# Performance work log

Hardware: AMD Instinct MI355X
Metric: run time of the kernel (lower is better)

## Reference

```python
import jax, jax.numpy as jnp
import numpy as np

IN_DIM = 300   # args.glove_init == 1
MID_DIM = 450  # ceil(1.5 * 300)
BATCH = 131072
NEG_SLOPE = 0.1


def setup_inputs() -> dict:
    key = jax.random.key(0)
    ks = jax.random.split(key, 13)

    def W(k, o, i):
        return jax.random.normal(k, (o, i), jnp.float32) * (1.0 / np.sqrt(i).astype(np.float32))

    def b(k, o):
        return jax.random.normal(k, (o,), jnp.float32) * 0.01

    inp = {"x": jax.random.normal(ks[0], (BATCH, IN_DIM), jnp.float32)}
    # NOT_op: Linear(300->450), LeakyReLU(0.1), Linear(450->300), LeakyReLU(0.1)
    inp["not_W1"] = W(ks[1], MID_DIM, IN_DIM);      inp["not_b1"] = b(ks[2], MID_DIM)
    inp["not_W2"] = W(ks[3], IN_DIM, MID_DIM);      inp["not_b2"] = b(ks[4], IN_DIM)
    # AND_op: Linear(600->450), LeakyReLU, Linear(450->300), LeakyReLU
    inp["and_W1"] = W(ks[5], MID_DIM, 2 * IN_DIM);  inp["and_b1"] = b(ks[6], MID_DIM)
    inp["and_W2"] = W(ks[7], IN_DIM, MID_DIM);      inp["and_b2"] = b(ks[8], IN_DIM)
    # OR_op: same shapes as AND_op
    inp["or_W1"] = W(ks[9], MID_DIM, 2 * IN_DIM);   inp["or_b1"] = b(ks[10], MID_DIM)
    inp["or_W2"] = W(ks[11], IN_DIM, MID_DIM);      inp["or_b2"] = b(ks[12], IN_DIM)
    inp["epoch"] = 1  # epoch <= el_epochs -> el_forward path
    return inp


def _mlp(x, W1, b1, W2, b2):
    # torch Linear: y = x @ W.T + b; LeakyReLU(0.1)
    h = jax.nn.leaky_relu(x @ W1.T + b1, NEG_SLOPE)
    return jax.nn.leaky_relu(h @ W2.T + b2, NEG_SLOPE)


def reference(x, not_W1, not_b1, not_W2, not_b2,
              and_W1, and_b1, and_W2, and_b2,
              or_W1, or_b1, or_W2, or_b2, epoch):
    # el_forward, fully batched (original loops over samples):
    # pairs: (x, NOT(NOT(x))), (x, AND([x,x])), (x, OR([x,x])); MSE over all pairs.
    s2a = _mlp(_mlp(x, not_W1, not_b1, not_W2, not_b2), not_W1, not_b1, not_W2, not_b2)
    xx = jnp.concatenate([x, x], axis=-1)  # [B, 600]
    s2b = _mlp(xx, and_W1, and_b1, and_W2, and_b2)
    s2c = _mlp(xx, or_W1, or_b1, or_W2, or_b2)
    # mean over the stacked 3B pairs == mean of the three per-pair MSEs
    loss = (jnp.mean((x - s2a) ** 2)
            + jnp.mean((x - s2b) ** 2)
            + jnp.mean((x - s2c) ** 2)) / 3.0
    return loss
```

## Files before the change

kernel.cpp:

```cpp
#include <hip/hip_runtime.h>

typedef __attribute__((ext_vector_type(8))) short short8;
typedef __attribute__((ext_vector_type(4))) float f32x4;

#define BATCH   131072
#define IND     300
#define MIDD    450
#define XS      328
#define HS      488
#define WXS     320
#define WHS     480
#define BM      96
#define NTHR    512
#define NBLK    ((BATCH + BM - 1) / BM)
#define MM      (BM / 16)

constexpr int SZ1 = 464 * WXS;
constexpr int SZ2 = 304 * WHS;
constexpr int O_NOT1 = 0;
constexpr int O_NOT2 = SZ1;
constexpr int O_AND1 = SZ1 + SZ2;
constexpr int O_AND2 = 2 * SZ1 + SZ2;
constexpr int O_OR1  = 2 * SZ1 + 2 * SZ2;
constexpr int O_OR2  = 3 * SZ1 + 2 * SZ2;
constexpr int WS_ELEMS = 3 * SZ1 + 3 * SZ2;

constexpr int XBYTES = BM * XS * 2;
constexpr int HBYTES = BM * HS * 2;
constexpr int LDS_BYTES = XBYTES + HBYTES;

__device__ __forceinline__ unsigned short f2b(float f) {
  unsigned u = __builtin_bit_cast(unsigned, f);
  u = (u + 0x7FFFu + ((u >> 16) & 1u)) >> 16;
  return (unsigned short)u;
}
__device__ __forceinline__ float b2f(unsigned short h) {
  unsigned u = ((unsigned)h) << 16;
  return __builtin_bit_cast(float, u);
}
__device__ __forceinline__ f32x4 mfma16(short8 a, short8 b, f32x4 c) {
  asm("v_mfma_f32_16x16x32_bf16 %0, %1, %2, %0" : "+v"(c) : "v"(a), "v"(b));
  return c;
}

__global__ void prep_weights(const float* __restrict__ nw1, const float* __restrict__ nw2,
                             const float* __restrict__ aw1, const float* __restrict__ aw2,
                             const float* __restrict__ ow1, const float* __restrict__ ow2,
                             unsigned short* __restrict__ ws)
{
  int idx = blockIdx.x * 256 + threadIdx.x;
  if (idx < 3 * SZ1) {
    int r = idx / SZ1, off = idx % SZ1;
    int n = off / WXS, k = off % WXS;
    float v = 0.f;
    if (n < MIDD && k < IND) {
      if (r == 0) v = nw1[n * IND + k];
      else {
        const float* s = (r == 1) ? aw1 : ow1;
        v = s[n * 2 * IND + k] + s[n * 2 * IND + IND + k];
      }
    }
    int base = (r == 0) ? O_NOT1 : (r == 1) ? O_AND1 : O_OR1;
    ws[base + off] = f2b(v);
  } else if (idx < WS_ELEMS) {
    int i2 = idx - 3 * SZ1;
    int r = i2 / SZ2, off = i2 % SZ2;
    int n = off / WHS, k = off % WHS;
    float v = 0.f;
    if (n < IND && k < MIDD) {
      const float* s = (r == 0) ? nw2 : (r == 1) ? aw2 : ow2;
      v = s[n * MIDD + k];
    }
    int base = (r == 0) ? O_NOT2 : (r == 1) ? O_AND2 : O_OR2;
    ws[base + off] = f2b(v);
  }
}

template <int KB, int NT, int N, bool MSE>
__device__ __forceinline__ void stage(const unsigned short* __restrict__ IN, int in_stride,
                                      const unsigned short* __restrict__ Wg, int wg_stride,
                                      const float* __restrict__ bias,
                                      unsigned short* __restrict__ Hout,
                                      const unsigned short* __restrict__ XT,
                                      float& sq, int rows, int tid, int wn, int l16, int lhi)
{
  constexpr int NJ = (NT + 7) / 8;
  f32x4 acc[MM][NJ];
#pragma unroll
  for (int m = 0; m < MM; m++)
#pragma unroll
    for (int j = 0; j < NJ; j++) acc[m][j] = f32x4{0.f, 0.f, 0.f, 0.f};

  const unsigned short* ap[MM];
#pragma unroll
  for (int m = 0; m < MM; m++) ap[m] = IN + (m * 16 + l16) * in_stride + lhi * 8;
  const unsigned short* bp[NJ];
#pragma unroll
  for (int j = 0; j < NJ; j++) {
    int nt = wn + 8 * j;
    int row = (nt < NT ? nt : 0) * 16 + l16;
    bp[j] = Wg + row * wg_stride + lhi * 8;
  }

  short8 a0[MM], a1[MM], b0[NJ], b1[NJ], b2[NJ];

#define LA_(buf, kk)                                                     \
  { _Pragma("unroll") for (int m = 0; m < MM; m++)                       \
      buf[m] = *(const short8*)(ap[m] + (kk) * 32); }
#define LB_(buf, kk)                                                     \
  { _Pragma("unroll") for (int j = 0; j < NJ; j++)                       \
      if (wn + 8 * j < NT) buf[j] = *(const short8*)(bp[j] + (kk) * 32); }

  LB_(b0, 0);
  LB_(b1, 1);
  LA_(a0, 0);

#pragma unroll
  for (int kb = 0; kb < KB; kb++) {
    short8* ac = (kb & 1) ? a1 : a0;
    short8* an = (kb & 1) ? a0 : a1;
    short8* bc = (kb % 3 == 0) ? b0 : (kb % 3 == 1) ? b1 : b2;
    short8* bn = ((kb + 2) % 3 == 0) ? b0 : ((kb + 2) % 3 == 1) ? b1 : b2;
    if (kb + 2 < KB) LB_(bn, kb + 2);
    if (kb + 1 < KB) LA_(an, kb + 1);
    __builtin_amdgcn_s_setprio(1);
#pragma unroll
    for (int j = 0; j < NJ; j++) {
      if (wn + 8 * j < NT) {
#pragma unroll
        for (int m = 0; m < MM; m++) acc[m][j] = mfma16(ac[m], bc[j], acc[m][j]);
      }
    }
    __builtin_amdgcn_s_setprio(0);
  }
#undef LA_
#undef LB_

  if (!MSE) __syncthreads();

#pragma unroll
  for (int j = 0; j < NJ; j++) {
    int nt = wn + 8 * j;
    if (nt >= NT) continue;
    int col = nt * 16 + l16;
    bool valid = col < N;
    float bv = valid ? bias[col] : 0.f;
#pragma unroll
    for (int m = 0; m < MM; m++) {
#pragma unroll
      for (int r = 0; r < 4; r++) {
        int row = m * 16 + lhi * 4 + r;
        float v = acc[m][j][r] + bv;
        v = v > 0.f ? v : 0.1f * v;
        if (MSE) {
          if (valid && row < rows) { float d = b2f(XT[row * XS + col]) - v; sq += d * d; }
        } else {
          if (valid) Hout[row * HS + col] = f2b(v);
        }
      }
    }
  }
  if (!MSE && N == IND) {
    for (int i = tid; i < BM * 20; i += NTHR) {
      int r = i / 20, c = i - r * 20;
      Hout[r * HS + IND + c] = 0;
    }
  }
}

__global__ __launch_bounds__(NTHR)
void fused(const float* __restrict__ x, const unsigned short* __restrict__ ws,
           const float* __restrict__ nb1, const float* __restrict__ nb2,
           const float* __restrict__ ab1, const float* __restrict__ ab2,
           const float* __restrict__ ob1, const float* __restrict__ ob2,
           float* __restrict__ out)
{
  extern __shared__ __align__(16) char smem[];
  unsigned short* X = (unsigned short*)smem;
  unsigned short* H = (unsigned short*)(smem + XBYTES);
  __shared__ float wsum[8];
  int tid = threadIdx.x, wid = tid >> 6, lane = tid & 63;
  int l16 = lane & 15, lhi = lane >> 4;

  for (int i = tid; i < LDS_BYTES / 4; i += NTHR) ((unsigned*)smem)[i] = 0u;
  __syncthreads();

  int row0 = blockIdx.x * BM;
  int rows = (row0 + BM <= BATCH) ? BM : (BATCH - row0);
  for (int i = tid; i < rows * IND; i += NTHR) {
    int r = i / IND, c = i - r * IND;
    X[r * XS + c] = f2b(x[(size_t)(row0 + r) * IND + c]);
  }
  __syncthreads();

  float sq = 0.f;
  stage<10, 29, MIDD, false>(X, XS, ws + O_NOT1, WXS, nb1, H, X, sq, rows, tid, wid, l16, lhi);
  __syncthreads();
  stage<15, 19, IND,  false>(H, HS, ws + O_NOT2, WHS, nb2, H, X, sq, rows, tid, wid, l16, lhi);
  __syncthreads();
  stage<10, 29, MIDD, false>(H, HS, ws + O_NOT1, WXS, nb1, H, X, sq, rows, tid, wid, l16, lhi);
  __syncthreads();
  stage<15, 19, IND,  true >(H, HS, ws + O_NOT2, WHS, nb2, H, X, sq, rows, tid, wid, l16, lhi);
  __syncthreads();
  stage<10, 29, MIDD, false>(X, XS, ws + O_AND1, WXS, ab1, H, X, sq, rows, tid, wid, l16, lhi);
  __syncthreads();
  stage<15, 19, IND,  true >(H, HS, ws + O_AND2, WHS, ab2, H, X, sq, rows, tid, wid, l16, lhi);
  __syncthreads();
  stage<10, 29, MIDD, false>(X, XS, ws + O_OR1,  WXS, ob1, H, X, sq, rows, tid, wid, l16, lhi);
  __syncthreads();
  stage<15, 19, IND,  true >(H, HS, ws + O_OR2,  WHS, ob2, H, X, sq, rows, tid, wid, l16, lhi);

#pragma unroll
  for (int off = 32; off > 0; off >>= 1) sq += __shfl_down(sq, off);
  if (lane == 0) wsum[wid] = sq;
  __syncthreads();
  if (tid == 0) {
    float s = 0.f;
#pragma unroll
    for (int w = 0; w < 8; w++) s += wsum[w];
    atomicAdd(out, s);
  }
}

__global__ void finalize(float* out) {
  out[0] *= (1.0f / (3.0f * (float)BATCH * (float)IND));
}

extern "C" void kernel_launch(void* const* d_in, const int* in_sizes, int n_in,
                              void* d_out, int out_size, void* d_ws, size_t ws_size,
                              hipStream_t stream) {
  const float* x   = (const float*)d_in[0];
  const float* nw1 = (const float*)d_in[1];
  const float* nb1 = (const float*)d_in[2];
  const float* nw2 = (const float*)d_in[3];
  const float* nb2 = (const float*)d_in[4];
  const float* aw1 = (const float*)d_in[5];
  const float* ab1 = (const float*)d_in[6];
  const float* aw2 = (const float*)d_in[7];
  const float* ab2 = (const float*)d_in[8];
  const float* ow1 = (const float*)d_in[9];
  const float* ob1 = (const float*)d_in[10];
  const float* ow2 = (const float*)d_in[11];
  const float* ob2 = (const float*)d_in[12];
  unsigned short* ws = (unsigned short*)d_ws;
  float* out = (float*)d_out;

  hipMemsetAsync(d_out, 0, sizeof(float), stream);

  int prep_blocks = (WS_ELEMS + 255) / 256;
  prep_weights<<<prep_blocks, 256, 0, stream>>>(nw1, nw2, aw1, aw2, ow1, ow2, ws);

  hipFuncSetAttribute((const void*)fused,
                      hipFuncAttributeMaxDynamicSharedMemorySize, LDS_BYTES);
  fused<<<NBLK, NTHR, LDS_BYTES, stream>>>(x, ws, nb1, nb2, ab1, ab2, ob1, ob2, out);

  finalize<<<1, 1, 0, stream>>>(out);
}
```

Before: 583.5 us.

## Drop LDS copy of x; load A operands directly from global fp32 and shrink tile

Removes the bf16 staging of the input x tile in LDS. First-layer A fragments are now read straight from global fp32 memory and converted to bf16 in registers, and the MSE step reads x from global as well. BM drops from 96 to 64, so LDS holds only the hidden buffer, which should allow more resident blocks. The cost is repeated uncoalesced global reads of x across three first layers and three MSE stages. The smaller tile also means less weight reuse per block.

```diff
diff --git a/kernel.cpp b/kernel.cpp
--- a/kernel.cpp
+++ b/kernel.cpp
@@ -6,13 +6,12 @@
 #define BATCH   131072
 #define IND     300
 #define MIDD    450
-#define XS      328
 #define HS      488
 #define WXS     320
 #define WHS     480
-#define BM      96
+#define BM      64
 #define NTHR    512
-#define NBLK    ((BATCH + BM - 1) / BM)
+#define NBLK    (BATCH / BM)
 #define MM      (BM / 16)
 
 constexpr int SZ1 = 464 * WXS;
@@ -25,9 +24,7 @@
 constexpr int O_OR2  = 3 * SZ1 + 2 * SZ2;
 constexpr int WS_ELEMS = 3 * SZ1 + 3 * SZ2;
 
-constexpr int XBYTES = BM * XS * 2;
-constexpr int HBYTES = BM * HS * 2;
-constexpr int LDS_BYTES = XBYTES + HBYTES;
+constexpr int LDS_BYTES = BM * HS * 2;
 
 __device__ __forceinline__ unsigned short f2b(float f) {
   unsigned u = __builtin_bit_cast(unsigned, f);
@@ -76,13 +73,13 @@
   }
 }
 
-template <int KB, int NT, int N, bool MSE>
-__device__ __forceinline__ void stage(const unsigned short* __restrict__ IN, int in_stride,
+template <int KB, int NT, int N, bool AFROMX, bool MSE>
+__device__ __forceinline__ void stage(const unsigned short* __restrict__ Hlds,
+                                      const float* __restrict__ xg,
                                       const unsigned short* __restrict__ Wg, int wg_stride,
                                       const float* __restrict__ bias,
                                       unsigned short* __restrict__ Hout,
-                                      const unsigned short* __restrict__ XT,
-                                      float& sq, int rows, int tid, int wn, int l16, int lhi)
+                                      float& sq, int tid, int wn, int l16, int lhi)
 {
   constexpr int NJ = (NT + 7) / 8;
   f32x4 acc[MM][NJ];
@@ -91,9 +88,13 @@
 #pragma unroll
     for (int j = 0; j < NJ; j++) acc[m][j] = f32x4{0.f, 0.f, 0.f, 0.f};
 
-  const unsigned short* ap[MM];
-#pragma unroll
-  for (int m = 0; m < MM; m++) ap[m] = IN + (m * 16 + l16) * in_stride + lhi * 8;
+  const unsigned short* ah[MM];
+  const float* ax[MM];
+#pragma unroll
+  for (int m = 0; m < MM; m++) {
+    ah[m] = Hlds + (m * 16 + l16) * HS + lhi * 8;
+    ax[m] = xg + (m * 16 + l16) * IND + lhi * 8;
+  }
   const unsigned short* bp[NJ];
 #pragma unroll
   for (int j = 0; j < NJ; j++) {
@@ -104,11 +105,29 @@
 
   short8 a0[MM], a1[MM], b0[NJ], b1[NJ], b2[NJ];
 
-#define LA_(buf, kk)                                                     \
-  { _Pragma("unroll") for (int m = 0; m < MM; m++)                       \
-      buf[m] = *(const short8*)(ap[m] + (kk) * 32); }
-#define LB_(buf, kk)                                                     \
-  { _Pragma("unroll") for (int j = 0; j < NJ; j++)                       \
+#define LA_(buf, kk)                                                          \
+  { _Pragma("unroll") for (int m = 0; m < MM; m++) {                          \
+      if (AFROMX) {                                                           \
+        if ((kk) == KB - 1) {        \
+          _Pragma("unroll") for (int i = 0; i < 8; i++) {                     \
+            int k = (kk) * 32 + lhi * 8 + i;                                  \
+            float v = (k < IND) ? ax[m][(kk) * 32 + i] : 0.f;                 \
+            buf[m][i] = (short)f2b(v);                                        \
+          }                                                                   \
+        } else {                                                              \
+          f32x4 f0 = *(const f32x4*)(ax[m] + (kk) * 32);                      \
+          f32x4 f1 = *(const f32x4*)(ax[m] + (kk) * 32 + 4);                  \
+          _Pragma("unroll") for (int i = 0; i < 4; i++) {                     \
+            buf[m][i]     = (short)f2b(f0[i]);                                \
+            buf[m][i + 4] = (short)f2b(f1[i]);                                \
+          }                                                                   \
+        }                                                                     \
+      } else {                                                                \
+        buf[m] = *(const short8*)(ah[m] + (kk) * 32);                         \
+      }                                                                       \
+    } }
+#define LB_(buf, kk)                                                          \
+  { _Pragma("unroll") for (int j = 0; j < NJ; j++)                            \
       if (wn + 8 * j < NT) buf[j] = *(const short8*)(bp[j] + (kk) * 32); }
 
   LB_(b0, 0);
@@ -153,7 +172,7 @@
         float v = acc[m][j][r] + bv;
         v = v > 0.f ? v : 0.1f * v;
         if (MSE) {
-          if (valid && row < rows) { float d = b2f(XT[row * XS + col]) - v; sq += d * d; }
+          if (valid) { float d = xg[row * IND + col] - v; sq += d * d; }
         } else {
           if (valid) Hout[row * HS + col] = f2b(v);
         }
@@ -176,8 +195,7 @@
            float* __restrict__ out)
 {
   extern __shared__ __align__(16) char smem[];
-  unsigned short* X = (unsigned short*)smem;
-  unsigned short* H = (unsigned short*)(smem + XBYTES);
+  unsigned short* H = (unsigned short*)smem;
   __shared__ float wsum[8];
   int tid = threadIdx.x, wid = tid >> 6, lane = tid & 63;
   int l16 = lane & 15, lhi = lane >> 4;
@@ -185,30 +203,24 @@
   for (int i = tid; i < LDS_BYTES / 4; i += NTHR) ((unsigned*)smem)[i] = 0u;
   __syncthreads();
 
-  int row0 = blockIdx.x * BM;
-  int rows = (row0 + BM <= BATCH) ? BM : (BATCH - row0);
-  for (int i = tid; i < rows * IND; i += NTHR) {
-    int r = i / IND, c = i - r * IND;
-    X[r * XS + c] = f2b(x[(size_t)(row0 + r) * IND + c]);
-  }
-  __syncthreads();
-
+  const float* xg = x + (size_t)blockIdx.x * BM * IND;
   float sq = 0.f;
-  stage<10, 29, MIDD, false>(X, XS, ws + O_NOT1, WXS, nb1, H, X, sq, rows, tid, wid, l16, lhi);
-  __syncthreads();
-  stage<15, 19, IND,  false>(H, HS, ws + O_NOT2, WHS, nb2, H, X, sq, rows, tid, wid, l16, lhi);
-  __syncthreads();
-  stage<10, 29, MIDD, false>(H, HS, ws + O_NOT1, WXS, nb1, H, X, sq, rows, tid, wid, l16, lhi);
-  __syncthreads();
-  stage<15, 19, IND,  true >(H, HS, ws + O_NOT2, WHS, nb2, H, X, sq, rows, tid, wid, l16, lhi);
-  __syncthreads();
-  stage<10, 29, MIDD, false>(X, XS, ws + O_AND1, WXS, ab1, H, X, sq, rows, tid, wid, l16, lhi);
-  __syncthreads();
-  stage<15, 19, IND,  true >(H, HS, ws + O_AND2, WHS, ab2, H, X, sq, rows, tid, wid, l16, lhi);
-  __syncthreads();
-  stage<10, 29, MIDD, false>(X, XS, ws + O_OR1,  WXS, ob1, H, X, sq, rows, tid, wid, l16, lhi);
-  __syncthreads();
-  stage<15, 19, IND,  true >(H, HS, ws + O_OR2,  WHS, ob2, H, X, sq, rows, tid, wid, l16, lhi);
+
+  stage<10, 29, MIDD, true,  false>(H, xg, ws + O_NOT1, WXS, nb1, H, sq, tid, wid, l16, lhi);
+  __syncthreads();
+  stage<15, 19, IND,  false, false>(H, xg, ws + O_NOT2, WHS, nb2, H, sq, tid, wid, l16, lhi);
+  __syncthreads();
+  stage<10, 29, MIDD, false, false>(H, xg, ws + O_NOT1, WXS, nb1, H, sq, tid, wid, l16, lhi);
+  __syncthreads();
+  stage<15, 19, IND,  false, true >(H, xg, ws + O_NOT2, WHS, nb2, H, sq, tid, wid, l16, lhi);
+  __syncthreads();
+  stage<10, 29, MIDD, true,  false>(H, xg, ws + O_AND1, WXS, ab1, H, sq, tid, wid, l16, lhi);
+  __syncthreads();
+  stage<15, 19, IND,  false, true >(H, xg, ws + O_AND2, WHS, ab2, H, sq, tid, wid, l16, lhi);
+  __syncthreads();
+  stage<10, 29, MIDD, true,  false>(H, xg, ws + O_OR1,  WXS, ob1, H, sq, tid, wid, l16, lhi);
+  __syncthreads();
+  stage<15, 19, IND,  false, true >(H, xg, ws + O_OR2,  WHS, ob2, H, sq, tid, wid, l16, lhi);
 
 #pragma unroll
   for (int off = 32; off > 0; off >>= 1) sq += __shfl_down(sq, off);
```

After: 1.058 ms. +81.3%, slower.
